# Kernel tuning notes

Hardware: AMD Instinct MI355X
Metric: run time of the kernel (lower is better)

The kernel has to match this reference:

```python
import jax, jax.numpy as jnp
import numpy as np

B, D, H, L_NS, L_S_DIM = 8, 512, 8, 64, 2048
HEAD_DIM = D // H


def setup_inputs() -> dict:
    key = jax.random.key(0)
    ks = jax.random.split(key, 12)
    L = L_S_DIM + L_NS
    x = jax.random.normal(ks[0], (B, L, D), jnp.float32)
    padding_mask = jax.random.randint(ks[1], (B, L_S_DIM), 0, 2, jnp.int32)
    s = 0.02
    params = {}
    for idx, name in enumerate(['wq', 'wk', 'wv']):
        params[name + '_sw'] = jax.random.normal(ks[2 + 3 * idx], (D, D), jnp.float32) * s
        params[name + '_sb'] = jnp.zeros((D,), jnp.float32)
        params[name + '_nw'] = jax.random.normal(ks[3 + 3 * idx], (L_NS, D, D), jnp.float32) * s
        params[name + '_nb'] = jnp.zeros((L_NS, D), jnp.float32)
    params['out_w'] = jax.random.normal(ks[11], (D, D), jnp.float32) * s
    params['out_b'] = jnp.zeros((D,), jnp.float32)
    return dict(x=x, padding_mask=padding_mask, L_s=2048, L_s_out=512, **params)


def mix_linear(x, L_s, sw, sb, nw, nb):
    # shared projection for first L_s tokens, token-specific weights for the rest
    out_s = x[:, :L_s] @ sw + sb                                # [B, L_s, D]
    out_ns = jnp.einsum('bni,nio->bno', x[:, L_s:], nw) + nb    # [B, L_ns, D]
    return jnp.concatenate([out_s, out_ns], axis=1)


def reference(x, padding_mask, L_s, L_s_out,
              wq_sw, wq_sb, wq_nw, wq_nb,
              wk_sw, wk_sb, wk_nw, wk_nb,
              wv_sw, wv_sb, wv_nw, wv_nb,
              out_w, out_b):
    Bb, L, d = x.shape
    L_ns = wq_nw.shape[0]
    hd = d // H
    K = mix_linear(x, L_s, wk_sw, wk_sb, wk_nw, wk_nb).reshape(Bb, L, H, hd).transpose(0, 2, 1, 3)
    V = mix_linear(x, L_s, wv_sw, wv_sb, wv_nw, wv_nb).reshape(Bb, L, H, hd).transpose(0, 2, 1, 3)
    if L_s_out < L_s:
        q_input = jnp.concatenate([x[:, L_s - L_s_out:L_s], x[:, L_s:]], axis=1)
    else:
        q_input = x
    L_q = L_s_out + L_ns
    L_k = L_s + L_ns
    Q = mix_linear(q_input, L_s_out, wq_sw, wq_sb, wq_nw, wq_nb).reshape(Bb, L_q, H, hd).transpose(0, 2, 1, 3)
    scores = jnp.einsum('bhqd,bhkd->bhqk', Q, K) / jnp.asarray(np.sqrt(hd), jnp.float32)
    i = jnp.arange(L_q)[:, None]
    j = jnp.arange(L_k)[None, :]
    causal = j <= i + (L_k - L_q)                                # [L_q, L_k]
    pad = jnp.concatenate([padding_mask.astype(bool), jnp.ones((Bb, L_ns), bool)], axis=1)
    mask = causal[None, None] & pad[:, None, None, :]            # [B, 1, L_q, L_k]
    scores = jnp.where(mask, scores, -1e9)
    w = jax.nn.softmax(scores, axis=-1)
    out = jnp.einsum('bhqk,bhkd->bhqd', w, V).transpose(0, 2, 1, 3).reshape(Bb, L_q, d)
    return out @ out_w + out_b
```

## Files before the change

kernel.cpp:

```cpp
#include <hip/hip_runtime.h>

typedef unsigned short u16;
typedef unsigned long long u64;
typedef short bf16x8 __attribute__((ext_vector_type(8)));
typedef float f32x4 __attribute__((ext_vector_type(4)));
typedef unsigned short u16x8 __attribute__((ext_vector_type(8)));

#define ATT_C (0.125f * 1.44269504088896340736f)

__device__ __forceinline__ u16 f2bf(float f) {
  unsigned u = __builtin_bit_cast(unsigned int, f);
  u += 0x7FFFu + ((u >> 16) & 1u);
  return (u16)(u >> 16);
}
__device__ __forceinline__ float bf2f(u16 u) {
  return __builtin_bit_cast(float, (unsigned)u << 16);
}
__device__ __forceinline__ void gload_lds16(const void* g, void* l) {
  __builtin_amdgcn_global_load_lds((__attribute__((address_space(1))) void*)(void*)g,
                                   (__attribute__((address_space(3))) void*)l, 16, 0, 0);
}

__global__ __launch_bounds__(256) void k_prep_pm(const int* __restrict__ pmask, u64* __restrict__ pbits) {
  int b = blockIdx.x;
  int t = threadIdx.x, w = t >> 6, l = t & 63;
  #pragma unroll
  for (int i = 0; i < 8; ++i) {
    int tile = i * 4 + w;
    u64 m = __ballot(pmask[b * 2048 + tile * 64 + l] != 0);
    if (l == 0) pbits[b * 32 + tile] = m;
  }
}

__global__ __launch_bounds__(256) void k_prep_x(const float* __restrict__ x, u16* __restrict__ xb) {
  int i = blockIdx.x * 256 + threadIdx.x;
  float4 v = reinterpret_cast<const float4*>(x)[i];
  ushort4 o;
  o.x = f2bf(v.x); o.y = f2bf(v.y); o.z = f2bf(v.z); o.w = f2bf(v.w);
  reinterpret_cast<ushort4*>(xb)[i] = o;
}

__global__ __launch_bounds__(256) void k_prep_wt(const float* __restrict__ w0, const float* __restrict__ w1,
                                                 const float* __restrict__ w2, const float* __restrict__ w3,
                                                 u16* __restrict__ wt) {
  __shared__ float Tl[64][65];
  int z = blockIdx.y;
  const float* W = (z == 0) ? w0 : (z == 1) ? w1 : (z == 2) ? w2 : w3;
  int kt = blockIdx.x >> 3, nt = blockIdx.x & 7;
  int t = threadIdx.x;
  int c = (t & 15) * 4, r0 = t >> 4;
  #pragma unroll
  for (int p = 0; p < 4; ++p) {
    int r = r0 + p * 16;
    float4 v = *reinterpret_cast<const float4*>(&W[(kt * 64 + r) * 512 + nt * 64 + c]);
    Tl[r][c] = v.x; Tl[r][c + 1] = v.y; Tl[r][c + 2] = v.z; Tl[r][c + 3] = v.w;
  }
  __syncthreads();
  #pragma unroll
  for (int p = 0; p < 4; ++p) {
    int n = r0 + p * 16;
    ushort4 u;
    u.x = f2bf(Tl[c + 0][n]); u.y = f2bf(Tl[c + 1][n]);
    u.z = f2bf(Tl[c + 2][n]); u.w = f2bf(Tl[c + 3][n]);
    *reinterpret_cast<ushort4*>(&wt[(z << 18) + (nt * 64 + n) * 512 + kt * 64 + c]) = u;
  }
}

__global__ __launch_bounds__(256) void k_nonshared(
    const float* __restrict__ x,
    const float* __restrict__ wq_nw, const float* __restrict__ wq_nb,
    const float* __restrict__ wk_nw, const float* __restrict__ wk_nb,
    const float* __restrict__ wv_nw, const float* __restrict__ wv_nb,
    u16* __restrict__ Qp, u16* __restrict__ Kp, u16* __restrict__ Vt) {
  int n = blockIdx.x, p = blockIdx.y;
  const float* W  = (p == 0) ? wq_nw : (p == 1) ? wk_nw : wv_nw;
  const float* bb = (p == 0) ? wq_nb : (p == 1) ? wk_nb : wv_nb;
  W += (long)n * 262144; bb += n * 512;
  __shared__ float As[4096];
  int t = threadIdx.x;
  #pragma unroll
  for (int i = 0; i < 4; ++i) {
    int f4 = t + i * 256;
    int bi = f4 >> 7;
    int off = (f4 & 127) * 4;
    reinterpret_cast<float4*>(As)[f4] =
        *reinterpret_cast<const float4*>(&x[(bi * 2112 + 2048 + n) * 512 + off]);
  }
  __syncthreads();
  int c4 = (t & 127) * 4, ih = t >> 7;
  float acc[8][4];
  #pragma unroll
  for (int b2 = 0; b2 < 8; ++b2) { acc[b2][0]=0.f; acc[b2][1]=0.f; acc[b2][2]=0.f; acc[b2][3]=0.f; }
  int i0 = ih * 256;
  #pragma unroll 4
  for (int i = i0; i < i0 + 256; ++i) {
    float4 wr = *reinterpret_cast<const float4*>(&W[i * 512 + c4]);
    #pragma unroll
    for (int b2 = 0; b2 < 8; ++b2) {
      float a = As[b2 * 512 + i];
      acc[b2][0] += a * wr.x; acc[b2][1] += a * wr.y;
      acc[b2][2] += a * wr.z; acc[b2][3] += a * wr.w;
    }
  }
  __syncthreads();
  if (ih == 1) {
    #pragma unroll
    for (int b2 = 0; b2 < 8; ++b2)
      reinterpret_cast<float4*>(As)[(t & 127) * 8 + b2] =
          make_float4(acc[b2][0], acc[b2][1], acc[b2][2], acc[b2][3]);
  }
  __syncthreads();
  if (ih == 0) {
    float4 bv = *reinterpret_cast<const float4*>(&bb[c4]);
    #pragma unroll
    for (int b2 = 0; b2 < 8; ++b2) {
      float4 o2 = reinterpret_cast<float4*>(As)[(t & 127) * 8 + b2];
      float r0 = acc[b2][0] + o2.x + bv.x, r1 = acc[b2][1] + o2.y + bv.y;
      float r2 = acc[b2][2] + o2.z + bv.z, r3 = acc[b2][3] + o2.w + bv.w;
      if (p == 0) {
        ushort4 u; u.x = f2bf(r0); u.y = f2bf(r1); u.z = f2bf(r2); u.w = f2bf(r3);
        *reinterpret_cast<ushort4*>(&Qp[(b2 * 576 + 512 + n) * 512 + c4]) = u;
      } else if (p == 1) {
        ushort4 u; u.x = f2bf(r0); u.y = f2bf(r1); u.z = f2bf(r2); u.w = f2bf(r3);
        *reinterpret_cast<ushort4*>(&Kp[(b2 * 2112 + 2048 + n) * 512 + c4]) = u;
      } else {
        Vt[(b2 * 512 + c4 + 0) * 2112 + 2048 + n] = f2bf(r0);
        Vt[(b2 * 512 + c4 + 1) * 2112 + 2048 + n] = f2bf(r1);
        Vt[(b2 * 512 + c4 + 2) * 2112 + 2048 + n] = f2bf(r2);
        Vt[(b2 * 512 + c4 + 3) * 2112 + 2048 + n] = f2bf(r3);
      }
    }
  }
}

template<int AMODE, int CMODE>
__global__ __launch_bounds__(256) void k_gemm(const u16* __restrict__ A, const u16* __restrict__ Wt,
                                              const float* __restrict__ bias, void* __restrict__ Cp,
                                              int mtpb, int arowoff, int cbs) {
  __shared__ u16 Al[4096];
  __shared__ u16 Wl[4096];
  int t = threadIdx.x, w = t >> 6, l = t & 63;
  int bm = blockIdx.x, n0 = blockIdx.y << 7;
  int batch = bm / mtpb, mt = bm % mtpb;
  int rowbase = batch * 2112 + arowoff + mt * 128;
  f32x4 zero = {0.f, 0.f, 0.f, 0.f};
  f32x4 acc[4][4];
  #pragma unroll
  for (int i = 0; i < 4; ++i)
    #pragma unroll
    for (int j = 0; j < 4; ++j) acc[i][j] = zero;
  int wm0 = (w >> 1) * 64, wn0 = (w & 1) * 64;
  int colL = l & 15, quad = l >> 4;
  for (int ks = 0; ks < 16; ++ks) {
    int k0 = ks * 32;
    #pragma unroll
    for (int hh = 0; hh < 2; ++hh) {
      int c = t + hh * 256;
      int r = c & 127, q = c >> 7;
      const u16* ga;
      if (AMODE == 0) ga = &A[(rowbase + r) * 512 + k0 + q * 8];
      else            ga = &A[((bm * 16 + ks) * 512 + c) * 8];
      gload_lds16(ga, &Al[c * 8]);
      gload_lds16(&Wt[(n0 + r) * 512 + k0 + q * 8], &Wl[c * 8]);
    }
    __syncthreads();
    bf16x8 af[4], bfr[4];
    #pragma unroll
    for (int mi = 0; mi < 4; ++mi)
      af[mi] = *reinterpret_cast<const bf16x8*>(&Al[(quad * 128 + wm0 + mi * 16 + colL) * 8]);
    #pragma unroll
    for (int ni = 0; ni < 4; ++ni)
      bfr[ni] = *reinterpret_cast<const bf16x8*>(&Wl[(quad * 128 + wn0 + ni * 16 + colL) * 8]);
    #pragma unroll
    for (int mi = 0; mi < 4; ++mi)
      #pragma unroll
      for (int ni = 0; ni < 4; ++ni)
        acc[mi][ni] = __builtin_amdgcn_mfma_f32_16x16x32_bf16(af[mi], bfr[ni], acc[mi][ni], 0, 0, 0);
    __syncthreads();
  }
  #pragma unroll
  for (int ni = 0; ni < 4; ++ni) {
    int n = n0 + wn0 + ni * 16 + colL;
    float bv = bias[n];
    #pragma unroll
    for (int mi = 0; mi < 4; ++mi) {
      int mbase = wm0 + mi * 16 + quad * 4;
      if (CMODE == 0) {
        u16* C = reinterpret_cast<u16*>(Cp);
        #pragma unroll
        for (int r = 0; r < 4; ++r)
          C[(batch * cbs + mt * 128 + mbase + r) * 512 + n] = f2bf(acc[mi][ni][r] + bv);
      } else if (CMODE == 1) {
        u16* C = reinterpret_cast<u16*>(Cp);
        int j0 = mt * 128 + mbase;
        ushort4 uv;
        uv.x = f2bf(acc[mi][ni][0] + bv); uv.y = f2bf(acc[mi][ni][1] + bv);
        uv.z = f2bf(acc[mi][ni][2] + bv); uv.w = f2bf(acc[mi][ni][3] + bv);
        *reinterpret_cast<ushort4*>(&C[(batch * 512 + n) * 2112 + j0]) = uv;
      } else {
        float* C = reinterpret_cast<float*>(Cp);
        #pragma unroll
        for (int r = 0; r < 4; ++r)
          C[(bm * 128 + mbase + r) * 512 + n] = acc[mi][ni][r] + bv;
      }
    }
  }
}

__global__ __launch_bounds__(256) void k_attn(const u16* __restrict__ Qp, const u16* __restrict__ Kp,
                                              const u16* __restrict__ Vt, const u64* __restrict__ pbits,
                                              u16* __restrict__ OPb, float* __restrict__ ML) {
  int qt = blockIdx.x, s = blockIdx.y, z = blockIdx.z;
  int b = z >> 3, h = z & 7;
  int T = qt + 25, Tq = (T + 2) / 3;
  int jt0 = s * Tq, jt1 = min(jt0 + Tq, T);
  int t = threadIdx.x, w = t >> 6, l = t & 63;
  int colL = l & 15, quad = l >> 4;
  __shared__ u16 PL[4][1024];
  u16* pw = PL[w];
  int qrow = b * 576 + qt * 64 + w * 16 + colL;
  bf16x8 qf[2];
  #pragma unroll
  for (int f = 0; f < 2; ++f)
    qf[f] = *reinterpret_cast<const bf16x8*>(&Qp[qrow * 512 + h * 64 + f * 32 + quad * 8]);
  f32x4 zero = {0.f, 0.f, 0.f, 0.f};
  f32x4 ov[4];
  #pragma unroll
  for (int i = 0; i < 4; ++i) ov[i] = zero;
  float m_run = -1.0e30f, l_run = 0.f;
  int i_q = qt * 64 + w * 16 + colL;
  const u16* Kb = Kp + (b * 2112) * 512 + h * 64;
  const u16* Vb = Vt + (b * 512 + h * 64) * 2112;
  for (int jt = jt0; jt < jt1; ++jt) {
    u64 pm = (jt < 32) ? pbits[b * 32 + jt] : ~0ULL;
    f32x4 st[4];
    #pragma unroll
    for (int mi = 0; mi < 4; ++mi) st[mi] = zero;
    #pragma unroll
    for (int mi = 0; mi < 4; ++mi) {
      const u16* kr = Kb + (jt * 64 + mi * 16 + colL) * 512;
      #pragma unroll
      for (int f = 0; f < 2; ++f) {
        bf16x8 kf = *reinterpret_cast<const bf16x8*>(&kr[f * 32 + quad * 8]);
        st[mi] = __builtin_amdgcn_mfma_f32_16x16x32_bf16(kf, qf[f], st[mi], 0, 0, 0);
      }
    }
    int thr = i_q + 1536 - jt * 64;
    float sv[4][4];
    float smax = -3.0e38f;
    #pragma unroll
    for (int mi = 0; mi < 4; ++mi)
      #pragma unroll
      for (int r = 0; r < 4; ++r) {
        int jl = mi * 16 + quad * 4 + r;
        bool ok = (jl <= thr) && (((pm >> jl) & 1ULL) != 0ULL);
        float sc = ok ? st[mi][r] : -3.0e38f;
        sv[mi][r] = sc;
        smax = fmaxf(smax, sc);
      }
    smax = fmaxf(smax, __shfl_xor(smax, 16));
    smax = fmaxf(smax, __shfl_xor(smax, 32));
    float m_new = fmaxf(m_run, smax);
    float alpha = exp2f((m_run - m_new) * ATT_C);
    float ls = 0.f;
    #pragma unroll
    for (int mi = 0; mi < 4; ++mi) {
      int o = mi * 2 + (quad >> 1);
      int jj0 = (quad & 1) * 4;
      float p0 = exp2f((sv[mi][0] - m_new) * ATT_C);
      float p1 = exp2f((sv[mi][1] - m_new) * ATT_C);
      float p2 = exp2f((sv[mi][2] - m_new) * ATT_C);
      float p3 = exp2f((sv[mi][3] - m_new) * ATT_C);
      ls += (p0 + p1) + (p2 + p3);
      unsigned u01 = (unsigned)f2bf(p0) | ((unsigned)f2bf(p1) << 16);
      unsigned u23 = (unsigned)f2bf(p2) | ((unsigned)f2bf(p3) << 16);
      *reinterpret_cast<unsigned*>(&pw[(o * 16 + colL) * 8 + jj0])     = u01;
      *reinterpret_cast<unsigned*>(&pw[(o * 16 + colL) * 8 + jj0 + 2]) = u23;
    }
    ls += __shfl_xor(ls, 16);
    ls += __shfl_xor(ls, 32);
    l_run = l_run * alpha + ls;
    m_run = m_new;
    float ar[4];
    #pragma unroll
    for (int r = 0; r < 4; ++r) ar[r] = __shfl(alpha, quad * 4 + r);
    #pragma unroll
    for (int ni = 0; ni < 4; ++ni)
      #pragma unroll
      for (int r = 0; r < 4; ++r) ov[ni][r] *= ar[r];
    #pragma unroll
    for (int f = 0; f < 2; ++f) {
      bf16x8 pf = *reinterpret_cast<const bf16x8*>(&pw[((f * 4 + quad) * 16 + colL) * 8]);
      #pragma unroll
      for (int ni = 0; ni < 4; ++ni) {
        bf16x8 vf = *reinterpret_cast<const bf16x8*>(
            &Vb[(ni * 16 + colL) * 2112 + jt * 64 + f * 32 + quad * 8]);
        ov[ni] = __builtin_amdgcn_mfma_f32_16x16x32_bf16(pf, vf, ov[ni], 0, 0, 0);
      }
    }
  }
  int pid = (qt * 3 + s) * 64 + z;
  u16* op = OPb + pid * 4096;
  #pragma unroll
  for (int ni = 0; ni < 4; ++ni)
    #pragma unroll
    for (int r = 0; r < 4; ++r)
      op[(w * 16 + quad * 4 + r) * 64 + ni * 16 + colL] = f2bf(ov[ni][r]);
  if (quad == 0) {
    ML[pid * 128 + w * 16 + colL] = m_run;
    ML[pid * 128 + 64 + w * 16 + colL] = l_run;
  }
}

__global__ __launch_bounds__(256) void k_attn_merge(const u16* __restrict__ OPb,
                                                    const float* __restrict__ ML,
                                                    u16* __restrict__ AO) {
  int blk = blockIdx.x;
  int qt = blk >> 6, z = blk & 63;
  int b = z >> 3, h = z & 7;
  int t = threadIdx.x;
  int q = t >> 2, g = t & 3;
  int pid0 = (qt * 3) * 64 + z;
  float m0 = ML[pid0 * 128 + q],         l0 = ML[pid0 * 128 + 64 + q];
  float m1 = ML[(pid0 + 64) * 128 + q],  l1 = ML[(pid0 + 64) * 128 + 64 + q];
  float m2 = ML[(pid0 + 128) * 128 + q], l2 = ML[(pid0 + 128) * 128 + 64 + q];
  float M = fmaxf(fmaxf(m0, m1), m2);
  float w0 = exp2f((m0 - M) * ATT_C);
  float w1 = exp2f((m1 - M) * ATT_C);
  float w2 = exp2f((m2 - M) * ATT_C);
  float rinv = 1.0f / (l0 * w0 + l1 * w1 + l2 * w2);
  w0 *= rinv; w1 *= rinv; w2 *= rinv;
  int R = b * 576 + qt * 64 + q;
  int obase = q * 64 + g * 16;
  #pragma unroll
  for (int hh = 0; hh < 2; ++hh) {
    int off = obase + hh * 8;
    u16x8 p0 = *reinterpret_cast<const u16x8*>(&OPb[pid0 * 4096 + off]);
    u16x8 p1 = *reinterpret_cast<const u16x8*>(&OPb[(pid0 + 64) * 4096 + off]);
    u16x8 p2 = *reinterpret_cast<const u16x8*>(&OPb[(pid0 + 128) * 4096 + off]);
    u16x8 o;
    #pragma unroll
    for (int i = 0; i < 8; ++i) {
      float v = bf2f(p0[i]) * w0 + bf2f(p1[i]) * w1 + bf2f(p2[i]) * w2;
      o[i] = f2bf(v);
    }
    int kk = h * 64 + g * 16 + hh * 8;
    int addr = ((((R >> 7) * 16 + (kk >> 5)) * 4 + ((kk >> 3) & 3)) << 10) + (R & 127) * 8;
    *reinterpret_cast<u16x8*>(&AO[addr]) = o;
  }
}

extern "C" void kernel_launch(void* const* d_in, const int* in_sizes, int n_in,
                              void* d_out, int out_size, void* d_ws, size_t ws_size,
                              hipStream_t stream) {
  const float* x     = (const float*)d_in[0];
  const int* pmask   = (const int*)d_in[1];
  const float* wq_sw = (const float*)d_in[4];
  const float* wq_sb = (const float*)d_in[5];
  const float* wq_nw = (const float*)d_in[6];
  const float* wq_nb = (const float*)d_in[7];
  const float* wk_sw = (const float*)d_in[8];
  const float* wk_sb = (const float*)d_in[9];
  const float* wk_nw = (const float*)d_in[10];
  const float* wk_nb = (const float*)d_in[11];
  const float* wv_sw = (const float*)d_in[12];
  const float* wv_sb = (const float*)d_in[13];
  const float* wv_nw = (const float*)d_in[14];
  const float* wv_nb = (const float*)d_in[15];
  const float* out_w = (const float*)d_in[16];
  const float* out_b = (const float*)d_in[17];

  char* ws = (char*)d_ws;
  u16* xb = (u16*)(ws);
  u16* OPb = (u16*)(ws);
  u16* wt = (u16*)(ws + 17301504);
  u16* Kp = (u16*)(ws + 19398656);
  u16* Vt = (u16*)(ws + 36700160);
  u16* Qp = (u16*)(ws + 54001664);
  u16* AO = (u16*)(ws + 58720256);
  u64* pbits = (u64*)d_out;
  float* ML = (float*)((char*)d_out + 4096);

  k_prep_pm<<<8, 256, 0, stream>>>(pmask, pbits);
  k_prep_x<<<8448, 256, 0, stream>>>(x, xb);
  k_prep_wt<<<dim3(64, 4), 256, 0, stream>>>(wq_sw, wk_sw, wv_sw, out_w, wt);
  k_nonshared<<<dim3(64, 3), 256, 0, stream>>>(x, wq_nw, wq_nb, wk_nw, wk_nb, wv_nw, wv_nb, Qp, Kp, Vt);
  k_gemm<0, 0><<<dim3(128, 4), 256, 0, stream>>>(xb, wt + 262144, wk_sb, (void*)Kp, 16, 0, 2112);
  k_gemm<0, 1><<<dim3(128, 4), 256, 0, stream>>>(xb, wt + 524288, wv_sb, (void*)Vt, 16, 0, 0);
  k_gemm<0, 0><<<dim3(32, 4), 256, 0, stream>>>(xb, wt, wq_sb, (void*)Qp, 4, 1536, 576);
  k_attn<<<dim3(9, 3, 64), 256, 0, stream>>>(Qp, Kp, Vt, pbits, OPb, ML);
  k_attn_merge<<<576, 256, 0, stream>>>(OPb, ML, AO);
  k_gemm<1, 2><<<dim3(36, 4), 256, 0, stream>>>(AO, wt + 786432, out_b, d_out, 1, 0, 0);
}
```

Baseline: 524.4 us.

## Stage K/V tiles in swizzled LDS with double-buffered async loads in attention

The attention kernel now copies each 64-key K and V tile into XOR-swizzled shared memory with global_load_lds, double-buffered so the next tile loads while the current one is computed. MFMA operands then come from LDS instead of scattered global reads. The PV product is computed transposed, so the per-row alpha rescale needs no shuffles. Partial outputs are normalised by l before storage, and the merge weights multiply by l to match. Also raises the unroll factor in the token-specific projection and packs the P stores into 64-bit writes. The cost is extra LDS and a block-wide barrier every iteration.

After: 520.4 us. Within noise of the previous version (-0.8%).

```diff
diff --git a/kernel.cpp b/kernel.cpp
--- a/kernel.cpp
+++ b/kernel.cpp
@@ -92,7 +92,7 @@
   #pragma unroll
   for (int b2 = 0; b2 < 8; ++b2) { acc[b2][0]=0.f; acc[b2][1]=0.f; acc[b2][2]=0.f; acc[b2][3]=0.f; }
   int i0 = ih * 256;
-  #pragma unroll 4
+  #pragma unroll 8
   for (int i = i0; i < i0 + 256; ++i) {
     float4 wr = *reinterpret_cast<const float4*>(&W[i * 512 + c4]);
     #pragma unroll
@@ -210,41 +210,70 @@
 __global__ __launch_bounds__(256) void k_attn(const u16* __restrict__ Qp, const u16* __restrict__ Kp,
                                               const u16* __restrict__ Vt, const u64* __restrict__ pbits,
                                               u16* __restrict__ OPb, float* __restrict__ ML) {
+  __shared__ u16 Kl[2][4096];
+  __shared__ u16 Vl[2][4096];
+  __shared__ u16 PL[4][1024];
   int qt = blockIdx.x, s = blockIdx.y, z = blockIdx.z;
   int b = z >> 3, h = z & 7;
   int T = qt + 25, Tq = (T + 2) / 3;
   int jt0 = s * Tq, jt1 = min(jt0 + Tq, T);
   int t = threadIdx.x, w = t >> 6, l = t & 63;
   int colL = l & 15, quad = l >> 4;
-  __shared__ u16 PL[4][1024];
   u16* pw = PL[w];
+  const u16* Kb = Kp + (b * 2112) * 512 + h * 64;
+  const u16* Vb = Vt + (b * 512 + h * 64) * 2112;
+  int sj0 = t >> 3, sq0 = (t & 7) ^ (sj0 & 7);
+  int sj1 = (t + 256) >> 3, sq1 = ((t + 256) & 7) ^ (sj1 & 7);
+
   int qrow = b * 576 + qt * 64 + w * 16 + colL;
   bf16x8 qf[2];
   #pragma unroll
   for (int f = 0; f < 2; ++f)
     qf[f] = *reinterpret_cast<const bf16x8*>(&Qp[qrow * 512 + h * 64 + f * 32 + quad * 8]);
   f32x4 zero = {0.f, 0.f, 0.f, 0.f};
-  f32x4 ov[4];
-  #pragma unroll
-  for (int i = 0; i < 4; ++i) ov[i] = zero;
+  f32x4 ovT[4];
+  #pragma unroll
+  for (int i = 0; i < 4; ++i) ovT[i] = zero;
   float m_run = -1.0e30f, l_run = 0.f;
   int i_q = qt * 64 + w * 16 + colL;
-  const u16* Kb = Kp + (b * 2112) * 512 + h * 64;
-  const u16* Vb = Vt + (b * 512 + h * 64) * 2112;
+
+  int fidx[4][2];
+  #pragma unroll
+  for (int mi = 0; mi < 4; ++mi)
+    #pragma unroll
+    for (int f = 0; f < 2; ++f)
+      fidx[mi][f] = (((mi * 16 + colL) * 8) + (((f * 4 + quad) ^ (colL & 7)))) * 8;
+
+  {
+    int jt = jt0;
+    gload_lds16(&Kb[(jt * 64 + sj0) * 512 + sq0 * 8], &Kl[0][t * 8]);
+    gload_lds16(&Kb[(jt * 64 + sj1) * 512 + sq1 * 8], &Kl[0][(t + 256) * 8]);
+    gload_lds16(&Vb[sj0 * 2112 + jt * 64 + sq0 * 8], &Vl[0][t * 8]);
+    gload_lds16(&Vb[sj1 * 2112 + jt * 64 + sq1 * 8], &Vl[0][(t + 256) * 8]);
+  }
+  int buf = 0;
   for (int jt = jt0; jt < jt1; ++jt) {
+    __syncthreads();
+    if (jt + 1 < jt1) {
+      int jn = jt + 1, nb = buf ^ 1;
+      gload_lds16(&Kb[(jn * 64 + sj0) * 512 + sq0 * 8], &Kl[nb][t * 8]);
+      gload_lds16(&Kb[(jn * 64 + sj1) * 512 + sq1 * 8], &Kl[nb][(t + 256) * 8]);
+      gload_lds16(&Vb[sj0 * 2112 + jn * 64 + sq0 * 8], &Vl[nb][t * 8]);
+      gload_lds16(&Vb[sj1 * 2112 + jn * 64 + sq1 * 8], &Vl[nb][(t + 256) * 8]);
+    }
+    const u16* Kc = Kl[buf];
+    const u16* Vc = Vl[buf];
     u64 pm = (jt < 32) ? pbits[b * 32 + jt] : ~0ULL;
     f32x4 st[4];
     #pragma unroll
     for (int mi = 0; mi < 4; ++mi) st[mi] = zero;
     #pragma unroll
-    for (int mi = 0; mi < 4; ++mi) {
-      const u16* kr = Kb + (jt * 64 + mi * 16 + colL) * 512;
+    for (int mi = 0; mi < 4; ++mi)
       #pragma unroll
       for (int f = 0; f < 2; ++f) {
-        bf16x8 kf = *reinterpret_cast<const bf16x8*>(&kr[f * 32 + quad * 8]);
+        bf16x8 kf = *reinterpret_cast<const bf16x8*>(&Kc[fidx[mi][f]]);
         st[mi] = __builtin_amdgcn_mfma_f32_16x16x32_bf16(kf, qf[f], st[mi], 0, 0, 0);
       }
-    }
     int thr = i_q + 1536 - jt * 64;
     float sv[4][4];
     float smax = -3.0e38f;
@@ -272,40 +301,39 @@
       float p2 = exp2f((sv[mi][2] - m_new) * ATT_C);
       float p3 = exp2f((sv[mi][3] - m_new) * ATT_C);
       ls += (p0 + p1) + (p2 + p3);
-      unsigned u01 = (unsigned)f2bf(p0) | ((unsigned)f2bf(p1) << 16);
-      unsigned u23 = (unsigned)f2bf(p2) | ((unsigned)f2bf(p3) << 16);
-      *reinterpret_cast<unsigned*>(&pw[(o * 16 + colL) * 8 + jj0])     = u01;
-      *reinterpret_cast<unsigned*>(&pw[(o * 16 + colL) * 8 + jj0 + 2]) = u23;
+      u64 pk = (u64)((unsigned)f2bf(p0) | ((unsigned)f2bf(p1) << 16)) |
+               ((u64)((unsigned)f2bf(p2) | ((unsigned)f2bf(p3) << 16)) << 32);
+      *reinterpret_cast<u64*>(&pw[(o * 16 + colL) * 8 + jj0]) = pk;
     }
     ls += __shfl_xor(ls, 16);
     ls += __shfl_xor(ls, 32);
     l_run = l_run * alpha + ls;
     m_run = m_new;
-    float ar[4];
-    #pragma unroll
-    for (int r = 0; r < 4; ++r) ar[r] = __shfl(alpha, quad * 4 + r);
-    #pragma unroll
-    for (int ni = 0; ni < 4; ++ni)
+    #pragma unroll
+    for (int mi = 0; mi < 4; ++mi)
       #pragma unroll
-      for (int r = 0; r < 4; ++r) ov[ni][r] *= ar[r];
+      for (int r = 0; r < 4; ++r) ovT[mi][r] *= alpha;
     #pragma unroll
     for (int f = 0; f < 2; ++f) {
-      bf16x8 pf = *reinterpret_cast<const bf16x8*>(&pw[((f * 4 + quad) * 16 + colL) * 8]);
+      bf16x8 pfB = *reinterpret_cast<const bf16x8*>(&pw[((f * 4 + quad) * 16 + colL) * 8]);
       #pragma unroll
-      for (int ni = 0; ni < 4; ++ni) {
-        bf16x8 vf = *reinterpret_cast<const bf16x8*>(
-            &Vb[(ni * 16 + colL) * 2112 + jt * 64 + f * 32 + quad * 8]);
-        ov[ni] = __builtin_amdgcn_mfma_f32_16x16x32_bf16(pf, vf, ov[ni], 0, 0, 0);
+      for (int mi = 0; mi < 4; ++mi) {
+        bf16x8 vA = *reinterpret_cast<const bf16x8*>(&Vc[fidx[mi][f]]);
+        ovT[mi] = __builtin_amdgcn_mfma_f32_16x16x32_bf16(vA, pfB, ovT[mi], 0, 0, 0);
       }
     }
-  }
+    buf ^= 1;
+  }
+  float linv = 1.0f / l_run;
   int pid = (qt * 3 + s) * 64 + z;
   u16* op = OPb + pid * 4096;
   #pragma unroll
-  for (int ni = 0; ni < 4; ++ni)
-    #pragma unroll
-    for (int r = 0; r < 4; ++r)
-      op[(w * 16 + quad * 4 + r) * 64 + ni * 16 + colL] = f2bf(ov[ni][r]);
+  for (int mi = 0; mi < 4; ++mi) {
+    ushort4 uv;
+    uv.x = f2bf(ovT[mi][0] * linv); uv.y = f2bf(ovT[mi][1] * linv);
+    uv.z = f2bf(ovT[mi][2] * linv); uv.w = f2bf(ovT[mi][3] * linv);
+    *reinterpret_cast<ushort4*>(&op[(w * 16 + colL) * 64 + mi * 16 + quad * 4]) = uv;
+  }
   if (quad == 0) {
     ML[pid * 128 + w * 16 + colL] = m_run;
     ML[pid * 128 + 64 + w * 16 + colL] = l_run;
@@ -325,10 +353,10 @@
   float m1 = ML[(pid0 + 64) * 128 + q],  l1 = ML[(pid0 + 64) * 128 + 64 + q];
   float m2 = ML[(pid0 + 128) * 128 + q], l2 = ML[(pid0 + 128) * 128 + 64 + q];
   float M = fmaxf(fmaxf(m0, m1), m2);
-  float w0 = exp2f((m0 - M) * ATT_C);
-  float w1 = exp2f((m1 - M) * ATT_C);
-  float w2 = exp2f((m2 - M) * ATT_C);
-  float rinv = 1.0f / (l0 * w0 + l1 * w1 + l2 * w2);
+  float w0 = exp2f((m0 - M) * ATT_C) * l0;
+  float w1 = exp2f((m1 - M) * ATT_C) * l1;
+  float w2 = exp2f((m2 - M) * ATT_C) * l2;
+  float rinv = 1.0f / (w0 + w1 + w2);
   w0 *= rinv; w1 *= rinv; w2 *= rinv;
   int R = b * 576 + qt * 64 + q;
   int obase = q * 64 + g * 16;
```
